# Optimization experiments

Measured on AMD Instinct MI355X. Metric: run time of the kernel, lower is better.

## Reference

```python
import jax, jax.numpy as jnp
import numpy as np

WS = 32      # window_size
P = 4        # patch size inside window
HEADS = 8
DIM_HEAD = 64
INNER = HEADS * DIM_HEAD  # 512
SCALE = DIM_HEAD ** -0.5


def setup_inputs() -> dict:
    key = jax.random.key(0)
    k1, k2, k3 = jax.random.split(key, 3)
    B, C, S = 8, 64, 256
    token_dim = P * P * C  # 1024
    x = jax.random.normal(k1, (B, C, S, S), dtype=jnp.float32)
    w_qkv = jax.random.normal(k2, (token_dim, 3 * INNER), dtype=jnp.float32) * (token_dim ** -0.5)
    w_out = jax.random.normal(k3, (INNER, token_dim), dtype=jnp.float32) * (INNER ** -0.5)
    b_out = jnp.zeros((token_dim,), dtype=jnp.float32)
    return {"x": x, "w_qkv": w_qkv, "w_out": w_out, "b_out": b_out}


def reference(x, w_qkv, w_out, b_out):
    B, C, H, W = x.shape
    H1, W1 = H // WS, W // WS
    # --- divide_regions: b c (h1 h) (w1 w) -> (b h1 w1) c h w ---
    xw = x.reshape(B, C, H1, WS, W1, WS).transpose(0, 2, 4, 1, 3, 5)
    xw = xw.reshape(B * H1 * W1, C, WS, WS)          # [n, C, ws, ws]
    n = xw.shape[0]
    nh = WS // P                                      # patches per side
    # patchify window: n c (nh p1) (nw p2) -> n (nh nw) (p1 p2 c)
    t = xw.reshape(n, C, nh, P, nh, P).transpose(0, 2, 4, 3, 5, 1)
    tokens = t.reshape(n, nh * nh, P * P * C)         # [n, T, D]
    # --- attention ---
    qkv = jnp.einsum('ntd,de->nte', tokens, w_qkv)    # [n, T, 3*inner]
    q, k, v = jnp.split(qkv, 3, axis=-1)
    def heads(a):
        return a.reshape(n, -1, HEADS, DIM_HEAD).transpose(0, 2, 1, 3)  # [n,h,T,dh]
    q, k, v = heads(q), heads(k), heads(v)
    attn = jax.nn.softmax(jnp.einsum('nhqd,nhkd->nhqk', q, k) * SCALE, axis=-1)
    o = jnp.einsum('nhqk,nhkd->nhqd', attn, v)        # [n,h,T,dh]
    o = o.transpose(0, 2, 1, 3).reshape(n, nh * nh, INNER)
    o = jnp.einsum('nte,ed->ntd', o, w_out) + b_out   # [n, T, D]
    # un-patchify: n (nh nw) (p1 p2 c) -> n c (nh p1) (nw p2)
    o = o.reshape(n, nh, nh, P, P, C).transpose(0, 5, 1, 3, 2, 4)
    o = o.reshape(n, C, WS, WS)
    # --- combine_regions: (b h1 w1) c h w -> b c (h1 h) (w1 w) ---
    o = o.reshape(B, H1, W1, C, WS, WS).transpose(0, 3, 1, 4, 2, 5)
    return o.reshape(B, C, H, W)
```

## Files before the change

### kernel.cpp

```cpp
#include <hip/hip_runtime.h>
#include <hip/hip_bf16.h>
#include <stdint.h>

typedef __attribute__((ext_vector_type(8))) short short8;
typedef __attribute__((ext_vector_type(4))) float floatx4;

constexpr int TD    = 1024;
constexpr int E3    = 1536;
constexpr int INNER = 512;
constexpr int NW    = 512;
constexpr int M_    = NW * 64;


constexpr size_t OFF_TOKA = 0;
constexpr size_t OFF_QKV  = (size_t)M_ * TD * 2;
constexpr size_t OFF_WQT  = OFF_QKV + (size_t)M_ * E3 * 2;
constexpr size_t OFF_WOT  = OFF_WQT + (size_t)E3 * TD * 2;
constexpr size_t OFF_BO   = OFF_WOT + (size_t)TD * INNER * 2;
constexpr size_t WS_NEED  = OFF_BO + TD * 4;

__device__ __forceinline__ void gl_lds16(const void* g, void* l) {
  __builtin_amdgcn_global_load_lds(
      (const __attribute__((address_space(1))) void*)g,
      (__attribute__((address_space(3))) void*)l, 16, 0, 0);
}

__global__ __launch_bounds__(256) void k_patchify(const float* __restrict__ x,
                                                  __hip_bfloat16* __restrict__ tokA) {
  __shared__ __hip_bfloat16 tok[8][1032];
  const int bid = blockIdx.x;
  const int n = bid >> 3, i = bid & 7;
  const int b = n >> 6, h1 = (n >> 3) & 7, w1 = n & 7;
  const int tid = threadIdx.x;
  for (int it = 0; it < 8; ++it) {
    int idx = it * 256 + tid;
    int w4 = idx & 7, p1 = (idx >> 3) & 3, c = idx >> 5;
    int h = h1 * 32 + i * 4 + p1;
    const float4 v = *(const float4*)&x[(((b * 64 + c) * 256 + h) * 256 + w1 * 32 + w4 * 4)];
    __hip_bfloat16* dst = &tok[w4][c * 16 + p1 * 4];
    dst[0] = __float2bfloat16(v.x);
    dst[1] = __float2bfloat16(v.y);
    dst[2] = __float2bfloat16(v.z);
    dst[3] = __float2bfloat16(v.w);
  }
  __syncthreads();
  for (int it = 0; it < 4; ++it) {
    int idx = it * 256 + tid;
    int ch = idx & 127, j = idx >> 7;
    uint4 v = *(const uint4*)&tok[j][ch * 8];
    *(uint4*)&tokA[(size_t)(n * 64 + i * 8 + j) * 1024 + ch * 8] = v;
  }
}

__global__ __launch_bounds__(256) void k_perm_wqkv(const float* __restrict__ wqkv,
                                                   __hip_bfloat16* __restrict__ wqT) {
  __shared__ __hip_bfloat16 wt[16][1032];
  const int e0 = blockIdx.x * 16, tid = threadIdx.x;
  for (int it = 0; it < 64; ++it) {
    int idx = it * 256 + tid;
    int e = idx & 15, d = idx >> 4;
    float v = wqkv[d * 1536 + e0 + e];
    int p1 = d >> 8, p2 = (d >> 6) & 3, c = d & 63;
    wt[e][c * 16 + p1 * 4 + p2] = __float2bfloat16(v);
  }
  __syncthreads();
  for (int it = 0; it < 8; ++it) {
    int idx = it * 256 + tid;
    int ch = idx & 127, e = idx >> 7;
    uint4 v = *(const uint4*)&wt[e][ch * 8];
    *(uint4*)&wqT[(size_t)(e0 + e) * 1024 + ch * 8] = v;
  }
}

__global__ __launch_bounds__(256) void k_perm_wout(const float* __restrict__ wout,
                                                   __hip_bfloat16* __restrict__ woT) {
  __shared__ __hip_bfloat16 wt[16][1032];
  const int e0 = blockIdx.x * 16, tid = threadIdx.x;
  for (int it = 0; it < 64; ++it) {
    int idx = it * 256 + tid;
    int d = idx & 1023, e = idx >> 10;
    float v = wout[(e0 + e) * 1024 + d];
    int p1 = d >> 8, p2 = (d >> 6) & 3, c = d & 63;
    wt[e][c * 16 + p1 * 4 + p2] = __float2bfloat16(v);
  }
  __syncthreads();
  for (int it = 0; it < 64; ++it) {
    int idx = it * 256 + tid;
    int e = idx & 15, dp = idx >> 4;
    woT[(size_t)dp * 512 + e0 + e] = wt[e][dp];
  }
}

__global__ __launch_bounds__(256) void k_perm_bias(const float* __restrict__ bout,
                                                   float* __restrict__ boP) {
  int dp = blockIdx.x * 256 + threadIdx.x;
  int c = dp >> 4, p1 = (dp >> 2) & 3, p2 = dp & 3;
  boP[dp] = bout[p1 * 256 + p2 * 64 + c];
}

template<int K>
__device__ __forceinline__ void gemm256_acc(
    const __hip_bfloat16* __restrict__ A,
    const __hip_bfloat16* __restrict__ Bt,
    int m0, int n0, int tid,
    __hip_bfloat16 (*As)[256][64], __hip_bfloat16 (*Bs)[256][64],
    floatx4 (&acc)[8][4])
{
  const int lane = tid & 63, wid = tid >> 6;
  const int wm = wid >> 2, wn = wid & 3;
  const int l15 = lane & 15, quad = lane >> 4;

  auto stageB = [&](int tile, int half, int buf) {
#pragma unroll
    for (int j = 0; j < 2; ++j) {
      int idx = j * 512 + tid;
      int rl = idx >> 3, slot = idx & 7;
      int r = half * 128 + rl;
      int ch = slot ^ (r & 7);
      gl_lds16(&Bt[(size_t)(n0 + r) * K + tile * 64 + ch * 8],
               (char*)&Bs[buf][0][0] + half * 16384 + idx * 16);
    }
  };
  auto stageA = [&](int tile, int chunk, int buf) {
#pragma unroll
    for (int j = 0; j < 2; ++j) {
      int rl = tid >> 3, slot = tid & 7;
      int r = j * 128 + chunk * 64 + rl;
      int ch = slot ^ (r & 7);
      gl_lds16(&A[(size_t)(m0 + r) * K + tile * 64 + ch * 8],
               (char*)&As[buf][0][0] + j * 16384 + chunk * 8192 + tid * 16);
    }
  };

  short8 bf[4][2];

#define PH(BUF, Q, STAGE, VMW)                                                    \
  do {                                                                            \
    short8 af[2][2];                                                              \
    _Pragma("unroll") for (int m2 = 0; m2 < 2; ++m2) {                            \
      const int r = wm * 128 + (2 * (Q) + m2) * 16 + l15;                         \
      _Pragma("unroll") for (int kh = 0; kh < 2; ++kh)                            \
        af[m2][kh] = *(const short8*)&As[BUF][r][((kh * 4 + quad) ^ (r & 7)) * 8];\
    }                                                                             \
    if ((Q) == 0) {                                                               \
      _Pragma("unroll") for (int n = 0; n < 4; ++n) {                             \
        const int rb = wn * 64 + n * 16 + l15;                                    \
        _Pragma("unroll") for (int kh = 0; kh < 2; ++kh)                          \
          bf[n][kh] = *(const short8*)&Bs[BUF][rb][((kh * 4 + quad) ^ (rb & 7)) * 8];\
      }                                                                           \
    }                                                                             \
    STAGE;                                                                        \
    __builtin_amdgcn_s_barrier();                                                 \
    asm volatile("s_waitcnt lgkmcnt(0)" ::: "memory");                            \
    __builtin_amdgcn_sched_barrier(0);                                            \
    __builtin_amdgcn_s_setprio(1);                                                \
    _Pragma("unroll") for (int kh = 0; kh < 2; ++kh)                              \
      _Pragma("unroll") for (int m2 = 0; m2 < 2; ++m2)                            \
        _Pragma("unroll") for (int n = 0; n < 4; ++n)                             \
          acc[2 * (Q) + m2][n] = __builtin_amdgcn_mfma_f32_16x16x32_bf16(         \
              af[m2][kh], bf[n][kh], acc[2 * (Q) + m2][n], 0, 0, 0);              \
    __builtin_amdgcn_s_setprio(0);                                                \
    __builtin_amdgcn_sched_barrier(0);                                            \
    VMW;                                                                          \
    __builtin_amdgcn_s_barrier();                                                 \
    __builtin_amdgcn_sched_barrier(0);                                            \
  } while (0)

  stageB(0, 0, 0); stageB(0, 1, 0); stageA(0, 0, 0); stageA(0, 1, 0);
  stageB(1, 0, 1); stageB(1, 1, 1); stageA(1, 0, 1);
  asm volatile("s_waitcnt vmcnt(6)" ::: "memory");
  __builtin_amdgcn_s_barrier();
  __builtin_amdgcn_sched_barrier(0);

  constexpr int NIT = K / 128;
#pragma unroll 1
  for (int i = 0; i < NIT - 1; ++i) {
    const int t1 = 2 * i + 1, t2 = 2 * i + 2, t3 = 2 * i + 3;
    PH(0, 0, stageA(t1, 1, 1), );
    PH(0, 1, stageB(t2, 0, 0), );
    PH(0, 2, stageB(t2, 1, 0), );
    PH(0, 3, stageA(t2, 0, 0), asm volatile("s_waitcnt vmcnt(6)" ::: "memory"));
    PH(1, 0, stageA(t2, 1, 0), );
    PH(1, 1, stageB(t3, 0, 1), );
    PH(1, 2, stageB(t3, 1, 1), );
    PH(1, 3, stageA(t3, 0, 1), asm volatile("s_waitcnt vmcnt(6)" ::: "memory"));
  }
  PH(0, 0, stageA(2 * NIT - 1, 1, 1), );
  PH(0, 1, , );
  PH(0, 2, , );
  PH(0, 3, , asm volatile("s_waitcnt vmcnt(0)" ::: "memory"));
  PH(1, 0, , );
  PH(1, 1, , );
  PH(1, 2, , );
  PH(1, 3, , );
#undef PH
}

__global__ __launch_bounds__(512) void k_gemm_qkv(const __hip_bfloat16* __restrict__ A,
                                                  const __hip_bfloat16* __restrict__ Bt,
                                                  __hip_bfloat16* __restrict__ Cmat) {
  __shared__ __hip_bfloat16 As[2][256][64];
  __shared__ __hip_bfloat16 Bs[2][256][64];
  const int tid = threadIdx.x;
  const int bid = blockIdx.x;
  const int swz = (bid & 7) * 96 + (bid >> 3);
  const int n0 = (swz % 6) * 256, m0 = (swz / 6) * 256;
  floatx4 acc[8][4] = {};
  gemm256_acc<1024>(A, Bt, m0, n0, tid, As, Bs, acc);
  const int lane = tid & 63, wid = tid >> 6;
  const int wm = wid >> 2, wn = wid & 3;
  const int l15 = lane & 15, quad = lane >> 4;
#pragma unroll
  for (int mt = 0; mt < 8; ++mt)
#pragma unroll
    for (int nt = 0; nt < 4; ++nt) {
      const int col = n0 + wn * 64 + nt * 16 + l15;
#pragma unroll
      for (int r = 0; r < 4; ++r) {
        const int row = m0 + wm * 128 + mt * 16 + quad * 4 + r;
        Cmat[(size_t)row * 1536 + col] = __float2bfloat16(acc[mt][nt][r]);
      }
    }
}

__global__ __launch_bounds__(256) void k_attn(const __hip_bfloat16* __restrict__ qkv,
                                              __hip_bfloat16* __restrict__ oattn) {
  __shared__ __hip_bfloat16 Qs[64 * 64];
  __shared__ __hip_bfloat16 Ks[64 * 64];
  __shared__ __hip_bfloat16 Vt[64 * 72];
  __shared__ __hip_bfloat16 Ps[64 * 72];
  const int win = blockIdx.x, head = blockIdx.y;
  const int tid = threadIdx.x, lane = tid & 63, wid = tid >> 6;
  const int l15 = lane & 15, quad = lane >> 4;
  const int sx = l15 & 7;
  const size_t base = (size_t)win * 64 * 1536 + head * 64;
  for (int l = 0; l < 2; ++l) {
    int idx = l * 256 + tid;
    int t = idx >> 3, ch = idx & 7;
    const size_t rowb = base + (size_t)t * 1536 + ch * 8;
    uint4 q = *(const uint4*)&qkv[rowb];
    uint4 k = *(const uint4*)&qkv[rowb + 512];
    uint4 v = *(const uint4*)&qkv[rowb + 1024];
    const int pos = (ch ^ (t & 7)) * 8;
    *(uint4*)&Qs[t * 64 + pos] = q;
    *(uint4*)&Ks[t * 64 + pos] = k;
    *(uint4*)&Ps[t * 64 + pos] = v;
  }
  __syncthreads();
  {
    const int t = tid & 63, w = tid >> 6;
#pragma unroll
    for (int jn = 0; jn < 2; ++jn) {
      int j = w * 2 + jn;
      short8 v = *(const short8*)&Ps[t * 64 + ((j ^ (t & 7)) * 8)];
#pragma unroll
      for (int jj = 0; jj < 8; ++jj) Vt[(j * 8 + jj) * 72 + t] = ((__hip_bfloat16*)&v)[jj];
    }
  }
  __syncthreads();
  floatx4 sacc[4] = {};
#pragma unroll
  for (int kk = 0; kk < 64; kk += 32) {
    const int pos = (((kk >> 3) + quad) ^ sx) * 8;
    short8 aq = *(const short8*)&Qs[(wid * 16 + l15) * 64 + pos];
#pragma unroll
    for (int ct = 0; ct < 4; ++ct) {
      short8 bk = *(const short8*)&Ks[(ct * 16 + l15) * 64 + pos];
      sacc[ct] = __builtin_amdgcn_mfma_f32_16x16x32_bf16(aq, bk, sacc[ct], 0, 0, 0);
    }
  }
#pragma unroll
  for (int ct = 0; ct < 4; ++ct)
#pragma unroll
    for (int r = 0; r < 4; ++r) sacc[ct][r] = sacc[ct][r] * 0.125f;
#pragma unroll
  for (int r = 0; r < 4; ++r) {
    float m = fmaxf(fmaxf(sacc[0][r], sacc[1][r]), fmaxf(sacc[2][r], sacc[3][r]));
    m = fmaxf(m, __shfl_xor(m, 1));
    m = fmaxf(m, __shfl_xor(m, 2));
    m = fmaxf(m, __shfl_xor(m, 4));
    m = fmaxf(m, __shfl_xor(m, 8));
    float ev[4]; float s0 = 0.f;
#pragma unroll
    for (int ct = 0; ct < 4; ++ct) { ev[ct] = __expf(sacc[ct][r] - m); s0 += ev[ct]; }
    s0 += __shfl_xor(s0, 1);
    s0 += __shfl_xor(s0, 2);
    s0 += __shfl_xor(s0, 4);
    s0 += __shfl_xor(s0, 8);
    float inv = 1.0f / s0;
    int row = wid * 16 + quad * 4 + r;
#pragma unroll
    for (int ct = 0; ct < 4; ++ct)
      Ps[row * 72 + ct * 16 + l15] = __float2bfloat16(ev[ct] * inv);
  }
  __syncthreads();
  floatx4 oacc[4] = {};
#pragma unroll
  for (int kk = 0; kk < 64; kk += 32) {
    const int q8 = quad * 8;
    short8 ap = *(const short8*)&Ps[(wid * 16 + l15) * 72 + kk + q8];
#pragma unroll
    for (int nt = 0; nt < 4; ++nt) {
      short8 bv = *(const short8*)&Vt[(nt * 16 + l15) * 72 + kk + q8];
      oacc[nt] = __builtin_amdgcn_mfma_f32_16x16x32_bf16(ap, bv, oacc[nt], 0, 0, 0);
    }
  }
#pragma unroll
  for (int nt = 0; nt < 4; ++nt) {
    int dh = nt * 16 + l15;
#pragma unroll
    for (int r = 0; r < 4; ++r) {
      int t = wid * 16 + quad * 4 + r;
      oattn[((size_t)win * 64 + t) * 512 + head * 64 + dh] = __float2bfloat16(oacc[nt][r]);
    }
  }
}

__global__ __launch_bounds__(512) void k_gemm_out(const __hip_bfloat16* __restrict__ A,
                                                  const __hip_bfloat16* __restrict__ Bt,
                                                  const float* __restrict__ bias,
                                                  float* __restrict__ out) {
  __shared__ __hip_bfloat16 As[2][256][64];
  __shared__ __hip_bfloat16 Bs[2][256][64];
  const int tid = threadIdx.x;
  const int bid = blockIdx.x;
  const int swz = (bid & 7) * 64 + (bid >> 3);
  const int n0 = (swz & 3) * 256, m0 = (swz >> 2) * 256;
  floatx4 acc[8][4] = {};
  gemm256_acc<512>(A, Bt, m0, n0, tid, As, Bs, acc);
  const int lane = tid & 63, wid = tid >> 6;
  const int wm = wid >> 2, wn = wid & 3;
  const int l15 = lane & 15, quad = lane >> 4;
#pragma unroll
  for (int nt = 0; nt < 4; ++nt) {
    const int dp = n0 + wn * 64 + nt * 16 + l15;
    const float bv = bias[dp];
    const int c = dp >> 4, p1 = (dp >> 2) & 3, p2 = dp & 3;
#pragma unroll
    for (int mt = 0; mt < 8; ++mt)
#pragma unroll
      for (int r = 0; r < 4; ++r) {
        const int m = m0 + wm * 128 + mt * 16 + quad * 4 + r;
        const int win = m >> 6, t = m & 63;
        const int i = t >> 3, j = t & 7;
        const int b = win >> 6, h1 = (win >> 3) & 7, w1 = win & 7;
        const int h = h1 * 32 + i * 4 + p1, w = w1 * 32 + j * 4 + p2;
        out[((b * 64 + c) * 256 + h) * 256 + w] = acc[mt][nt][r] + bv;
      }
  }
}

extern "C" void kernel_launch(void* const* d_in, const int* in_sizes, int n_in,
                              void* d_out, int out_size, void* d_ws, size_t ws_size,
                              hipStream_t stream) {
  const float* x    = (const float*)d_in[0];
  const float* wqkv = (const float*)d_in[1];
  const float* wout = (const float*)d_in[2];
  const float* bout = (const float*)d_in[3];
  float* out = (float*)d_out;
  char* ws = (char*)d_ws;
  if (ws_size < WS_NEED) return;

  __hip_bfloat16* tokA  = (__hip_bfloat16*)(ws + OFF_TOKA);
  __hip_bfloat16* oattn = (__hip_bfloat16*)(ws + OFF_TOKA);
  __hip_bfloat16* qkv   = (__hip_bfloat16*)(ws + OFF_QKV);
  __hip_bfloat16* wqT   = (__hip_bfloat16*)(ws + OFF_WQT);
  __hip_bfloat16* woT   = (__hip_bfloat16*)(ws + OFF_WOT);
  float* boP = (float*)(ws + OFF_BO);

  k_perm_wqkv<<<96, 256, 0, stream>>>(wqkv, wqT);
  k_perm_wout<<<32, 256, 0, stream>>>(wout, woT);
  k_perm_bias<<<4, 256, 0, stream>>>(bout, boP);
  k_patchify<<<4096, 256, 0, stream>>>(x, tokA);
  k_gemm_qkv<<<768, 512, 0, stream>>>(tokA, wqT, qkv);
  k_attn<<<dim3(512, 8), 256, 0, stream>>>(qkv, oattn);
  k_gemm_out<<<512, 512, 0, stream>>>(oattn, woT, boP, out);
}
```

Before: 443.6 us.

## Double-buffer A fragments across GEMM phases and precompute staging base pointers

Restructures the shared GEMM mainloop so the A-operand LDS fragments for the next phase load while the current phase's MFMAs run, using a two-slot register buffer. This removes the full lgkmcnt(0) wait before each MFMA block. It also hoists the address arithmetic for the global-to-LDS staging into precomputed base pointers, adjusts where the vmcnt waits sit, and adds a min-blocks-per-CU hint of 2 to both GEMM kernels. The extra fragment registers and the occupancy hint could raise register pressure or cause spills, and dropping the explicit LDS wait relies on the compiler inserting the correct waits.

```diff
diff --git a/kernel.cpp b/kernel.cpp
--- a/kernel.cpp
+++ b/kernel.cpp
@@ -110,55 +110,55 @@
   const int wm = wid >> 2, wn = wid & 3;
   const int l15 = lane & 15, quad = lane >> 4;
 
+  const int rl8 = tid >> 3;
+  const int ch0 = (tid & 7) ^ (rl8 & 7);
+  const __hip_bfloat16* Abase = A  + (size_t)(m0 + rl8) * K + ch0 * 8;
+  const __hip_bfloat16* Bbase = Bt + (size_t)(n0 + rl8) * K + ch0 * 8;
+
   auto stageB = [&](int tile, int half, int buf) {
 #pragma unroll
-    for (int j = 0; j < 2; ++j) {
-      int idx = j * 512 + tid;
-      int rl = idx >> 3, slot = idx & 7;
-      int r = half * 128 + rl;
-      int ch = slot ^ (r & 7);
-      gl_lds16(&Bt[(size_t)(n0 + r) * K + tile * 64 + ch * 8],
-               (char*)&Bs[buf][0][0] + half * 16384 + idx * 16);
-    }
+    for (int j = 0; j < 2; ++j)
+      gl_lds16(Bbase + (size_t)(half * 128 + j * 64) * K + tile * 64,
+               (char*)&Bs[buf][0][0] + half * 16384 + (j * 512 + tid) * 16);
   };
   auto stageA = [&](int tile, int chunk, int buf) {
 #pragma unroll
-    for (int j = 0; j < 2; ++j) {
-      int rl = tid >> 3, slot = tid & 7;
-      int r = j * 128 + chunk * 64 + rl;
-      int ch = slot ^ (r & 7);
-      gl_lds16(&A[(size_t)(m0 + r) * K + tile * 64 + ch * 8],
+    for (int j = 0; j < 2; ++j)
+      gl_lds16(Abase + (size_t)(j * 128 + chunk * 64) * K + tile * 64,
                (char*)&As[buf][0][0] + j * 16384 + chunk * 8192 + tid * 16);
-    }
   };
 
+  short8 af[2][2][2];
   short8 bf[4][2];
 
-#define PH(BUF, Q, STAGE, VMW)                                                    \
+#define VM6 asm volatile("s_waitcnt vmcnt(6)" ::: "memory")
+#define VM0 asm volatile("s_waitcnt vmcnt(0)" ::: "memory")
+
+#define PH(CS, QC, BUFC, LDB, QN, BUFN, PFAF, STAGE, VMW)                         \
   do {                                                                            \
-    short8 af[2][2];                                                              \
-    _Pragma("unroll") for (int m2 = 0; m2 < 2; ++m2) {                            \
-      const int r = wm * 128 + (2 * (Q) + m2) * 16 + l15;                         \
-      _Pragma("unroll") for (int kh = 0; kh < 2; ++kh)                            \
-        af[m2][kh] = *(const short8*)&As[BUF][r][((kh * 4 + quad) ^ (r & 7)) * 8];\
-    }                                                                             \
-    if ((Q) == 0) {                                                               \
+    if (LDB) {                                                                    \
       _Pragma("unroll") for (int n = 0; n < 4; ++n) {                             \
         const int rb = wn * 64 + n * 16 + l15;                                    \
         _Pragma("unroll") for (int kh = 0; kh < 2; ++kh)                          \
-          bf[n][kh] = *(const short8*)&Bs[BUF][rb][((kh * 4 + quad) ^ (rb & 7)) * 8];\
+          bf[n][kh] = *(const short8*)&Bs[BUFC][rb][((kh * 4 + quad) ^ (rb & 7)) * 8]; \
+      }                                                                           \
+    }                                                                             \
+    if (PFAF) {                                                                   \
+      _Pragma("unroll") for (int m2 = 0; m2 < 2; ++m2) {                          \
+        const int r = wm * 128 + (2 * (QN) + m2) * 16 + l15;                      \
+        _Pragma("unroll") for (int kh = 0; kh < 2; ++kh)                          \
+          af[(CS) ^ 1][m2][kh] = *(const short8*)&As[BUFN][r][((kh * 4 + quad) ^ (r & 7)) * 8]; \
       }                                                                           \
     }                                                                             \
     STAGE;                                                                        \
     __builtin_amdgcn_s_barrier();                                                 \
-    asm volatile("s_waitcnt lgkmcnt(0)" ::: "memory");                            \
     __builtin_amdgcn_sched_barrier(0);                                            \
     __builtin_amdgcn_s_setprio(1);                                                \
     _Pragma("unroll") for (int kh = 0; kh < 2; ++kh)                              \
       _Pragma("unroll") for (int m2 = 0; m2 < 2; ++m2)                            \
         _Pragma("unroll") for (int n = 0; n < 4; ++n)                             \
-          acc[2 * (Q) + m2][n] = __builtin_amdgcn_mfma_f32_16x16x32_bf16(         \
-              af[m2][kh], bf[n][kh], acc[2 * (Q) + m2][n], 0, 0, 0);              \
+          acc[2 * (QC) + m2][n] = __builtin_amdgcn_mfma_f32_16x16x32_bf16(        \
+              af[CS][m2][kh], bf[n][kh], acc[2 * (QC) + m2][n], 0, 0, 0);         \
     __builtin_amdgcn_s_setprio(0);                                                \
     __builtin_amdgcn_sched_barrier(0);                                            \
     VMW;                                                                          \
@@ -168,37 +168,49 @@
 
   stageB(0, 0, 0); stageB(0, 1, 0); stageA(0, 0, 0); stageA(0, 1, 0);
   stageB(1, 0, 1); stageB(1, 1, 1); stageA(1, 0, 1);
-  asm volatile("s_waitcnt vmcnt(6)" ::: "memory");
+  VM6;
   __builtin_amdgcn_s_barrier();
   __builtin_amdgcn_sched_barrier(0);
+#pragma unroll
+  for (int m2 = 0; m2 < 2; ++m2) {
+    const int r = wm * 128 + m2 * 16 + l15;
+#pragma unroll
+    for (int kh = 0; kh < 2; ++kh)
+      af[0][m2][kh] = *(const short8*)&As[0][r][((kh * 4 + quad) ^ (r & 7)) * 8];
+  }
 
   constexpr int NIT = K / 128;
 #pragma unroll 1
   for (int i = 0; i < NIT - 1; ++i) {
     const int t1 = 2 * i + 1, t2 = 2 * i + 2, t3 = 2 * i + 3;
-    PH(0, 0, stageA(t1, 1, 1), );
-    PH(0, 1, stageB(t2, 0, 0), );
-    PH(0, 2, stageB(t2, 1, 0), );
-    PH(0, 3, stageA(t2, 0, 0), asm volatile("s_waitcnt vmcnt(6)" ::: "memory"));
-    PH(1, 0, stageA(t2, 1, 0), );
-    PH(1, 1, stageB(t3, 0, 1), );
-    PH(1, 2, stageB(t3, 1, 1), );
-    PH(1, 3, stageA(t3, 0, 1), asm volatile("s_waitcnt vmcnt(6)" ::: "memory"));
-  }
-  PH(0, 0, stageA(2 * NIT - 1, 1, 1), );
-  PH(0, 1, , );
-  PH(0, 2, , );
-  PH(0, 3, , asm volatile("s_waitcnt vmcnt(0)" ::: "memory"));
-  PH(1, 0, , );
-  PH(1, 1, , );
-  PH(1, 2, , );
-  PH(1, 3, , );
+    PH(0, 0, 0, 1, 1, 0, 1, stageA(t1, 1, 1), VM6);
+    PH(1, 1, 0, 0, 2, 0, 1, stageB(t2, 0, 0), );
+    PH(0, 2, 0, 0, 3, 0, 1, stageB(t2, 1, 0), VM6);
+    PH(1, 3, 0, 0, 0, 1, 1, stageA(t2, 0, 0), );
+    PH(0, 0, 1, 1, 1, 1, 1, stageA(t2, 1, 0), VM6);
+    PH(1, 1, 1, 0, 2, 1, 1, stageB(t3, 0, 1), );
+    PH(0, 2, 1, 0, 3, 1, 1, stageB(t3, 1, 1), VM6);
+    PH(1, 3, 1, 0, 0, 0, 1, stageA(t3, 0, 1), );
+  }
+  {
+    const int tE = 2 * NIT - 1;
+    PH(0, 0, 0, 1, 1, 0, 1, stageA(tE, 1, 1), VM6);
+    PH(1, 1, 0, 0, 2, 0, 1, , );
+    PH(0, 2, 0, 0, 3, 0, 1, , VM0);
+    PH(1, 3, 0, 0, 0, 1, 1, , );
+    PH(0, 0, 1, 1, 1, 1, 1, , );
+    PH(1, 1, 1, 0, 2, 1, 1, , );
+    PH(0, 2, 1, 0, 3, 1, 1, , );
+    PH(1, 3, 1, 0, 0, 0, 0, , );
+  }
 #undef PH
-}
-
-__global__ __launch_bounds__(512) void k_gemm_qkv(const __hip_bfloat16* __restrict__ A,
-                                                  const __hip_bfloat16* __restrict__ Bt,
-                                                  __hip_bfloat16* __restrict__ Cmat) {
+#undef VM6
+#undef VM0
+}
+
+__global__ __launch_bounds__(512, 2) void k_gemm_qkv(const __hip_bfloat16* __restrict__ A,
+                                                     const __hip_bfloat16* __restrict__ Bt,
+                                                     __hip_bfloat16* __restrict__ Cmat) {
   __shared__ __hip_bfloat16 As[2][256][64];
   __shared__ __hip_bfloat16 Bs[2][256][64];
   const int tid = threadIdx.x;
@@ -316,10 +328,10 @@
   }
 }
 
-__global__ __launch_bounds__(512) void k_gemm_out(const __hip_bfloat16* __restrict__ A,
-                                                  const __hip_bfloat16* __restrict__ Bt,
-                                                  const float* __restrict__ bias,
-                                                  float* __restrict__ out) {
+__global__ __launch_bounds__(512, 2) void k_gemm_out(const __hip_bfloat16* __restrict__ A,
+                                                     const __hip_bfloat16* __restrict__ Bt,
+                                                     const float* __restrict__ bias,
+                                                     float* __restrict__ out) {
   __shared__ __hip_bfloat16 As[2][256][64];
   __shared__ __hip_bfloat16 Bs[2][256][64];
   const int tid = threadIdx.x;
```

New measurement: 444.7 us. About the same (+0.3%).
